# Kernel tuning notes

Measured on AMD Instinct MI355X. Metric: run time of the kernel, lower is better.

## Reference

```python
import math
import jax, jax.numpy as jnp
from jax import lax
import numpy as np

B, N, D, H, L, F = 128, 200, 128, 8, 3, 2048


def setup_inputs():
    key = jax.random.key(0)
    ks = jax.random.split(key, 24)
    g = lambda i, shape: (0.05 * jax.random.normal(ks[i], shape)).astype(jnp.float32)
    coords = jax.random.uniform(ks[0], (B, N, 2), dtype=jnp.float32)
    demands = jax.random.uniform(ks[1], (B, N), minval=1.0, maxval=10.0, dtype=jnp.float32)
    demands = demands.at[:, 0].set(0.0)  # depot demand = 0
    capacity = jnp.full((B,), 50.0, jnp.float32)
    return dict(
        coords=coords, demands_raw=demands, capacity_raw=capacity,
        embed_W=g(2, (D, 3)), embed_b=g(3, (D,)),
        Wqkv=g(4, (L, 3 * D, D)), bqkv=g(5, (L, 3 * D)),
        Wo=g(6, (L, D, D)), bo=g(7, (L, D)),
        W1=g(8, (L, F, D)), b1=g(9, (L, F)),
        W2=g(10, (L, D, F)), b2=g(11, (L, D)),
        ln1_g=jnp.ones((L, D), jnp.float32), ln1_b=jnp.zeros((L, D), jnp.float32),
        ln2_g=jnp.ones((L, D), jnp.float32), ln2_b=jnp.zeros((L, D), jnp.float32),
        Wq=g(12, (D, D)), Wk=g(13, (D, D)),
        Wcap=g(14, (D, 1)), bcap=g(15, (D,)),
        Wctx=g(16, (D, 3 * D)), bctx=g(17, (D,)),
    )


def _ln(x, g, b):
    m = x.mean(-1, keepdims=True)
    v = ((x - m) ** 2).mean(-1, keepdims=True)
    return (x - m) / jnp.sqrt(v + 1e-5) * g + b


def _forward(coords, demands_raw, capacity_raw, embed_W, embed_b, Wqkv, bqkv, Wo, bo,
             W1, b1, W2, b2, ln1_g, ln1_b, ln2_g, ln2_b, Wq, Wk, Wcap, bcap, Wctx, bctx):
    Bd, Nd, _ = coords.shape
    cap = capacity_raw.reshape(Bd, 1)
    demand_ratio = demands_raw / cap                       # (B,N)
    x = jnp.concatenate([coords, demand_ratio[..., None]], -1)  # (B,N,3)
    h = x @ embed_W.T + embed_b                            # (B,N,D)
    d = h.shape[-1]
    dh = d // H
    # --- transformer encoder (post-LN, relu FFN), eval mode (no dropout) ---
    for i in range(Wqkv.shape[0]):
        qkv = h @ Wqkv[i].T + bqkv[i]
        q, k, v = jnp.split(qkv, 3, -1)
        q = q.reshape(Bd, Nd, H, dh)
        k = k.reshape(Bd, Nd, H, dh)
        v = v.reshape(Bd, Nd, H, dh)
        s = jnp.einsum('bqhd,bkhd->bhqk', q, k) / math.sqrt(dh)
        a = jax.nn.softmax(s, -1)
        o = jnp.einsum('bhqk,bkhd->bqhd', a, v).reshape(Bd, Nd, d) @ Wo[i].T + bo[i]
        h = _ln(h + o, ln1_g[i], ln1_b[i])
        f = jax.nn.relu(h @ W1[i].T + b1[i]) @ W2[i].T + b2[i]
        h = _ln(h + f, ln2_g[i], ln2_b[i])
    global_ctx = h.mean(1)                                 # (B,D)
    kmat = h @ Wk.T                                        # K cache: static across steps
    sqrt_d = math.sqrt(d)
    max_steps = 2 * (Nd - 1) + 1
    ar = jnp.arange(Bd)

    def step(carry, _):
        current, visited, remaining, done, key = carry
        key, sk = jax.random.split(key)
        cur_h = h[ar, current]                             # (B,D)
        cap_h = remaining @ Wcap.T + bcap                  # (B,D)
        q_in = jnp.concatenate([cur_h, global_ctx, cap_h], -1)
        q = (q_in @ Wctx.T + bctx) @ Wq.T                  # (B,D)
        logits = (kmat * q[:, None, :]).sum(-1) / sqrt_d   # (B,N)
        infeasible = visited | (demand_ratio > remaining)
        feas_cust = (~visited[:, 1:]) & (demand_ratio[:, 1:] <= remaining)
        has_feas = feas_cust.any(1)
        all_served = visited[:, 1:].all(1)
        force_depot = all_served & (current != 0) & (~done)
        at_depot = (current == 0) & (~done)
        not_depot = (current != 0) & (~done)
        # prevent_early_return=True path
        depot_mask = (at_depot & has_feas) | (not_depot & has_feas & (~all_served))
        infeasible = infeasible.at[:, 0].set(infeasible[:, 0] | depot_mask)
        force_depot = force_depot | (not_depot & (~has_feas)) | done
        masked = jnp.where(infeasible, -1e9, logits)
        logp = jax.nn.log_softmax(masked, -1)
        sel = jax.random.categorical(sk, masked)           # sampling decode
        sel_logp = logp[ar, sel]
        sel = jnp.where(force_depot, 0, sel)
        sel_logp = jnp.where(force_depot, 0.0, sel_logp)
        is_depot = sel == 0
        take = demand_ratio[ar, sel][:, None]
        remaining = jnp.clip(jnp.where(is_depot[:, None], 1.0, remaining - take), 0.0, 1.0)
        visited = visited.at[ar, sel].set(visited[ar, sel] | (~is_depot))
        done = done | (visited[:, 1:].all(1) & (sel == 0))
        return (sel, visited, remaining, done, key), (sel, sel_logp)

    init = (jnp.zeros(Bd, jnp.int32), jnp.zeros((Bd, Nd), bool),
            jnp.ones((Bd, 1), coords.dtype), jnp.zeros(Bd, bool), jax.random.key(42))
    _, (acts, lps) = lax.scan(step, init, None, length=max_steps)
    path = jnp.concatenate([jnp.zeros((Bd, 1), jnp.int32), acts.T], 1)  # (B, 1+max_steps)
    logps = lps.sum(0)                                                  # (B,)
    return path, logps


def reference(coords, demands_raw, capacity_raw, embed_W, embed_b, Wqkv, bqkv, Wo, bo,
              W1, b1, W2, b2, ln1_g, ln1_b, ln2_g, ln2_b, Wq, Wk, Wcap, bcap, Wctx, bctx):
    return _forward(coords, demands_raw, capacity_raw, embed_W, embed_b, Wqkv, bqkv, Wo, bo,
                    W1, b1, W2, b2, ln1_g, ln1_b, ln2_g, ln2_b, Wq, Wk, Wcap, bcap, Wctx, bctx)
```

## Files before the change

### kernel.cpp

```cpp
#include <hip/hip_runtime.h>
#include <hip/hip_bf16.h>
#include <stdint.h>
#include <math.h>

#define NB 128
#define NN 200
#define ND 128
#define NH 8
#define DH 16
#define NL 3
#define NF 2048
#define NT (NB * NN)
#define NSTEP 399

__host__ __device__ inline void tf2x32(unsigned k0, unsigned k1, unsigned x0, unsigned x1,
                                       unsigned* o0, unsigned* o1) {
  unsigned ks[3] = {k0, k1, k0 ^ k1 ^ 0x1BD11BDAu};
  x0 += ks[0]; x1 += ks[1];
  const unsigned R[2][4] = {{13u, 15u, 26u, 6u}, {17u, 29u, 16u, 24u}};
#pragma unroll
  for (int i = 0; i < 5; ++i) {
#pragma unroll
    for (int j = 0; j < 4; ++j) {
      unsigned r = R[i & 1][j];
      x0 += x1;
      x1 = (x1 << r) | (x1 >> (32u - r));
      x1 ^= x0;
    }
    x0 += ks[(i + 1) % 3];
    x1 += ks[(i + 2) % 3] + (unsigned)(i + 1);
  }
  *o0 = x0; *o1 = x1;
}

__global__ void k_rng(unsigned* __restrict__ rng) {
  __shared__ unsigned ksh[2 * NSTEP];
  const int l = threadIdx.x;
  if (l == 0) {
    unsigned k0 = 0u, k1 = 42u;
    for (int t = 0; t < NSTEP; ++t) {
      ksh[2 * t] = k0; ksh[2 * t + 1] = k1;
      unsigned a0, a1;
      tf2x32(k0, k1, 0u, 0u, &a0, &a1);
      k0 = a0; k1 = a1;
    }
  }
  __syncthreads();
  for (int t = l; t < NSTEP; t += 64) {
    unsigned s0, s1;
    tf2x32(ksh[2 * t], ksh[2 * t + 1], 0u, 1u, &s0, &s1);
    rng[2 * t] = s0; rng[2 * t + 1] = s1;
  }
}

__global__ __launch_bounds__(256) void k_gum(const unsigned* __restrict__ rng, float* __restrict__ gum) {
  int idx = blockIdx.x * 256 + threadIdx.x;
  if (idx >= NSTEP * NT) return;
  int t = idx / NT, j = idx - t * NT;
  unsigned o0, o1;
  tf2x32(rng[2 * t], rng[2 * t + 1], 0u, (unsigned)j, &o0, &o1);
  unsigned bits = o0 ^ o1;
  float u01 = __uint_as_float((bits >> 9) | 0x3f800000u) - 1.0f;
  float uu = fmaxf(1.17549435082228751e-38f, u01);
  gum[idx] = (float)(-log(-log((double)uu)));
}

__global__ void k_tr(const float* __restrict__ src, float* __restrict__ dst, int R, int C) {
  int i = blockIdx.x * 256 + threadIdx.x;
  if (i >= R * C) return;
  int c = i / R, r = i - c * R;
  dst[i] = src[(size_t)r * C + c];
}

__global__ void k_trd(const float* __restrict__ src, double* __restrict__ dst, int R, int C) {
  int i = blockIdx.x * 256 + threadIdx.x;
  if (i >= R * C) return;
  int c = i / R, r = i - c * R;
  dst[i] = (double)src[(size_t)r * C + c];
}

__global__ void k_embed(const float* __restrict__ coords, const float* __restrict__ dem,
                        const float* __restrict__ cap, const float* __restrict__ eW,
                        const float* __restrict__ eb, float* __restrict__ h, float* __restrict__ dr) {
  int gid = blockIdx.x * blockDim.x + threadIdx.x;
  int t = gid >> 7, d = gid & 127;
  int b = t / NN;
  float drv = dem[t] / cap[b];
  double acc = (double)eW[d * 3] * (double)coords[2 * t]
             + (double)eW[d * 3 + 1] * (double)coords[2 * t + 1]
             + (double)eW[d * 3 + 2] * (double)drv;
  h[gid] = (float)acc + eb[d];
  if (d == 0) dr[t] = drv;
}

#define QT 8
__global__ __launch_bounds__(384) void k_qkv(const float* __restrict__ h, const double* __restrict__ WT,
                                             const float* __restrict__ bias, float* __restrict__ qkv) {
  const int t0 = blockIdx.x * QT, j = threadIdx.x;
  __shared__ double hsh[ND][QT];
  for (int idx = j; idx < ND * QT; idx += 384) {
    int t = idx & 7, k = idx >> 3;
    hsh[k][t] = (double)h[(size_t)(t0 + t) * ND + k];
  }
  __syncthreads();
  double acc[QT];
#pragma unroll
  for (int t = 0; t < QT; ++t) acc[t] = 0.0;
  for (int k = 0; k < ND; ++k) {
    double w = WT[(size_t)k * 384 + j];
#pragma unroll
    for (int t = 0; t < QT; ++t) acc[t] += w * hsh[k][t];
  }
  float bv = bias[j];
#pragma unroll
  for (int t = 0; t < QT; ++t)
    qkv[(size_t)(t0 + t) * 384 + j] = (float)acc[t] + bv;
}

__global__ __launch_bounds__(256) void k_attn(const float* __restrict__ qkv, float* __restrict__ att) {
  const int b = blockIdx.x / NH, hh = blockIdx.x % NH, tid = threadIdx.x;
  const int lane = tid & 63, w = tid >> 6;
  __shared__ float qsh[NN][DH + 1];
  __shared__ float ksh[NN][DH + 1];
  __shared__ float vsh[NN][DH + 1];
  __shared__ float ashw[4][NN + 8];
  for (int idx = tid; idx < NN * DH; idx += 256) {
    int n = idx / DH, d2 = idx % DH;
    size_t base = (size_t)(b * NN + n) * 384 + hh * DH + d2;
    qsh[n][d2] = qkv[base];
    ksh[n][d2] = qkv[base + ND];
    vsh[n][d2] = qkv[base + 2 * ND];
  }
  __syncthreads();
  const int dd = lane & 15, q4 = lane >> 4;
  for (int qn = w; qn < NN; qn += 4) {
    double qv[DH];
#pragma unroll
    for (int d = 0; d < DH; ++d) qv[d] = (double)qsh[qn][d];
    float sf[4];
#pragma unroll
    for (int s = 0; s < 4; ++s) {
      int n = lane + 64 * s;
      if (n < NN) {
        double a = 0.0;
#pragma unroll
        for (int d = 0; d < DH; ++d) a += qv[d] * (double)ksh[n][d];
        sf[s] = (float)a / 4.0f;
      } else sf[s] = -3.0e38f;
    }
    float m = fmaxf(fmaxf(sf[0], sf[1]), fmaxf(sf[2], sf[3]));
    for (int off = 1; off < 64; off <<= 1) m = fmaxf(m, __shfl_xor(m, off, 64));
    double e[4];
    double esum = 0.0;
#pragma unroll
    for (int s = 0; s < 4; ++s) {
      int n = lane + 64 * s;
      e[s] = (n < NN) ? exp((double)(sf[s] - m)) : 0.0;
      esum += e[s];
    }
    for (int off = 1; off < 64; off <<= 1) esum += __shfl_xor(esum, off, 64);
#pragma unroll
    for (int s = 0; s < 4; ++s) {
      int n = lane + 64 * s;
      if (n < NN) ashw[w][n] = (float)(e[s] / esum);
    }
    double o = 0.0;
    for (int i = 0; i < 50; ++i) {
      int n = q4 * 50 + i;
      o += (double)ashw[w][n] * (double)vsh[n][dd];
    }
    o += __shfl_xor(o, 16, 64);
    o += __shfl_xor(o, 32, 64);
    if (lane < DH)
      att[(size_t)(b * NN + qn) * ND + hh * DH + lane] = (float)o;
  }
}

#define OT 4
__global__ __launch_bounds__(128) void k_oln(const float* __restrict__ att, const double* __restrict__ WoT,
                                             const float* __restrict__ bo, const float* __restrict__ g,
                                             const float* __restrict__ bb, float* __restrict__ h) {
  const int t0 = blockIdx.x * OT, d = threadIdx.x;
  __shared__ double ash[ND][OT];
  __shared__ float xsh[OT][ND];
  __shared__ float mred[OT], sred[OT];
  for (int idx = d; idx < ND * OT; idx += 128) {
    int t = idx & 3, k = idx >> 2;
    ash[k][t] = (double)att[(size_t)(t0 + t) * ND + k];
  }
  __syncthreads();
  double acc[OT];
#pragma unroll
  for (int t = 0; t < OT; ++t) acc[t] = 0.0;
  for (int k = 0; k < ND; ++k) {
    double w = WoT[(size_t)k * ND + d];
#pragma unroll
    for (int t = 0; t < OT; ++t) acc[t] += w * ash[k][t];
  }
  float bv = bo[d];
#pragma unroll
  for (int t = 0; t < OT; ++t) {
    float o = (float)acc[t] + bv;
    xsh[t][d] = h[(size_t)(t0 + t) * ND + d] + o;
  }
  __syncthreads();
  if (d < OT) {
    double sv = 0.0;
    for (int k = 0; k < ND; ++k) sv += (double)xsh[d][k];
    float m = (float)(sv / 128.0);
    double sq = 0.0;
    for (int k = 0; k < ND; ++k) { float tf = xsh[d][k] - m; sq += (double)tf * (double)tf; }
    mred[d] = m;
    sred[d] = sqrtf((float)(sq / 128.0) + 1e-5f);
  }
  __syncthreads();
#pragma unroll
  for (int t = 0; t < OT; ++t) {
    float tf = xsh[t][d] - mred[t];
    h[(size_t)(t0 + t) * ND + d] = tf / sred[t] * g[d] + bb[d];
  }
}

#define FT 8
#define JC 1024
__global__ __launch_bounds__(256) void k_ffn(float* __restrict__ h, const double* __restrict__ W1T,
                                             const float* __restrict__ b1, const float* __restrict__ W2T,
                                             const float* __restrict__ b2, const float* __restrict__ g,
                                             const float* __restrict__ bb) {
  const int t0 = blockIdx.x * FT, tid = threadIdx.x;
  __shared__ double hsh[ND][FT];
  __shared__ double fsh_raw[FT * JC / 2];
  __shared__ float xsh[FT][ND];
  __shared__ float mred[FT], sred[FT];
  float* fshf = (float*)fsh_raw;
  for (int idx = tid; idx < ND * FT; idx += 256) {
    int t = idx & 7, k = idx >> 3;
    hsh[k][t] = (double)h[(size_t)(t0 + t) * ND + k];
  }
  __syncthreads();
  const int jg = tid >> 5, dl = tid & 31;
  double acc2[4][FT];
#pragma unroll
  for (int a = 0; a < 4; ++a)
#pragma unroll
    for (int t = 0; t < FT; ++t) acc2[a][t] = 0.0;
  for (int c = 0; c < 2; ++c) {
    {
      const int j0 = tid * 4;
      double acc[4][FT];
#pragma unroll
      for (int a = 0; a < 4; ++a)
#pragma unroll
        for (int t = 0; t < FT; ++t) acc[a][t] = 0.0;
      const double* wp0 = W1T + (size_t)c * JC + j0;
      double2 wa = *(const double2*)wp0;
      double2 wb = *(const double2*)(wp0 + 2);
      for (int k = 0; k < ND; ++k) {
        double wd[4] = {wa.x, wa.y, wb.x, wb.y};
        const double* wn = W1T + (size_t)((k + 1) & 127) * NF + c * JC + j0;
        wa = *(const double2*)wn;
        wb = *(const double2*)(wn + 2);
        double hv[FT];
#pragma unroll
        for (int t = 0; t < FT; ++t) hv[t] = hsh[k][t];
#pragma unroll
        for (int a = 0; a < 4; ++a)
#pragma unroll
          for (int t = 0; t < FT; ++t) acc[a][t] += wd[a] * hv[t];
      }
#pragma unroll
      for (int a = 0; a < 4; ++a) {
        float bv = b1[c * JC + j0 + a];
#pragma unroll
        for (int t = 0; t < FT; ++t) {
          float f = (float)acc[a][t] + bv;
          fshf[t * JC + j0 + a] = fmaxf(f, 0.0f);
        }
      }
    }
    __syncthreads();
    {
      float4 wv = *(const float4*)(W2T + (size_t)(c * JC + ((jg << 7) | (jg & 127))) * ND + (dl << 2));
      for (int i = 0; i < 128; ++i) {
        int jj = (jg << 7) | ((i + jg) & 127);
        int jn = (jg << 7) | ((i + 1 + jg) & 127);
        float4 wnext = *(const float4*)(W2T + (size_t)(c * JC + jn) * ND + (dl << 2));
        double fv[FT];
#pragma unroll
        for (int t = 0; t < FT; ++t) fv[t] = (double)fshf[t * JC + jj];
        double wd[4] = {(double)wv.x, (double)wv.y, (double)wv.z, (double)wv.w};
#pragma unroll
        for (int a = 0; a < 4; ++a)
#pragma unroll
          for (int t = 0; t < FT; ++t) acc2[a][t] += wd[a] * fv[t];
        wv = wnext;
      }
    }
    __syncthreads();
  }
  double* red = fsh_raw;
  for (int half = 0; half < 2; ++half) {
    if (half) __syncthreads();
#pragma unroll
    for (int a = 0; a < 4; ++a)
#pragma unroll
      for (int t = 0; t < 4; ++t)
        red[((jg * 4 + t) << 7) + (dl << 2) + a] = acc2[a][half * 4 + t];
    __syncthreads();
    for (int idx = tid; idx < ND * 4; idx += 256) {
      int t = idx >> 7, d = idx & 127;
      double s = 0.0;
#pragma unroll
      for (int jg2 = 0; jg2 < 8; ++jg2) s += red[((jg2 * 4 + t) << 7) + d];
      float o = (float)s + b2[d];
      int tt = half * 4 + t;
      xsh[tt][d] = (float)hsh[d][tt] + o;
    }
  }
  __syncthreads();
  if (tid < FT) {
    double sv = 0.0;
    for (int d = 0; d < ND; ++d) sv += (double)xsh[tid][d];
    float m = (float)(sv / 128.0);
    double sq = 0.0;
    for (int d = 0; d < ND; ++d) { float tf = xsh[tid][d] - m; sq += (double)tf * (double)tf; }
    mred[tid] = m;
    sred[tid] = sqrtf((float)(sq / 128.0) + 1e-5f);
  }
  __syncthreads();
  for (int idx = tid; idx < ND * FT; idx += 256) {
    int d = idx & 127, t = idx >> 7;
    float tf = xsh[t][d] - mred[t];
    h[(size_t)(t0 + t) * ND + d] = tf / sred[t] * g[d] + bb[d];
  }
}

__global__ __launch_bounds__(128) void k_gctx(const float* __restrict__ h, float* __restrict__ gctx) {
  int b = blockIdx.x, d = threadIdx.x;
  double acc = 0.0;
  for (int n = 0; n < NN; ++n) acc += (double)h[(size_t)(b * NN + n) * ND + d];
  gctx[b * ND + d] = (float)(acc / 200.0);
}

#define KT 8
__global__ __launch_bounds__(128) void k_kmat(const float* __restrict__ h, const double* __restrict__ WkT,
                                              float* __restrict__ kmat) {
  const int t0 = blockIdx.x * KT, d = threadIdx.x;
  __shared__ double hsh[ND][KT];
  for (int idx = d; idx < ND * KT; idx += 128) {
    int t = idx & 7, k = idx >> 3;
    hsh[k][t] = (double)h[(size_t)(t0 + t) * ND + k];
  }
  __syncthreads();
  double acc[KT];
#pragma unroll
  for (int t = 0; t < KT; ++t) acc[t] = 0.0;
  for (int k = 0; k < ND; ++k) {
    double w = WkT[(size_t)k * ND + d];
#pragma unroll
    for (int t = 0; t < KT; ++t) acc[t] += w * hsh[k][t];
  }
#pragma unroll
  for (int t = 0; t < KT; ++t)
    kmat[(size_t)(t0 + t) * ND + d] = (float)acc[t];
}

__global__ __launch_bounds__(128) void k_prep1(const float* __restrict__ Wctx, const float* __restrict__ bcap,
                                               const float* __restrict__ Wcap, const float* __restrict__ bctx,
                                               double* __restrict__ t1, double* __restrict__ wu) {
  int k = threadIdx.x;
  double a = 0.0, c = 0.0;
  for (int m = 0; m < ND; ++m) {
    double wc = (double)Wctx[(size_t)k * 384 + 256 + m];
    a += wc * (double)bcap[m];
    c += wc * (double)Wcap[m];
  }
  t1[k] = a + (double)bctx[k];
  wu[k] = c;
}

__global__ __launch_bounds__(128) void k_M(const float* __restrict__ Wq, const float* __restrict__ Wctx,
                                           double* __restrict__ M) {
  int d = blockIdx.x, j = threadIdx.x;
  double acc = 0.0;
  for (int k = 0; k < ND; ++k)
    acc += (double)Wq[(size_t)d * ND + k] * (double)Wctx[(size_t)k * 384 + j];
  M[(size_t)d * ND + j] = acc;
}

__global__ __launch_bounds__(128) void k_u(const float* __restrict__ Wq, const double* __restrict__ wu,
                                           double* __restrict__ u) {
  int d = threadIdx.x;
  double acc = 0.0;
  for (int k = 0; k < ND; ++k) acc += (double)Wq[(size_t)d * ND + k] * wu[k];
  u[d] = acc;
}

__global__ __launch_bounds__(128) void k_t2(const float* __restrict__ Wctx, const float* __restrict__ gctx,
                                            double* __restrict__ t2) {
  int b = blockIdx.x, k = threadIdx.x;
  double acc = 0.0;
  for (int m = 0; m < ND; ++m)
    acc += (double)Wctx[(size_t)k * 384 + 128 + m] * (double)gctx[b * ND + m];
  t2[(size_t)b * ND + k] = acc;
}

__global__ __launch_bounds__(128) void k_vb(const float* __restrict__ Wq, const double* __restrict__ t2,
                                            const double* __restrict__ t1, double* __restrict__ vb) {
  int b = blockIdx.x, d = threadIdx.x;
  double acc = 0.0;
  for (int k = 0; k < ND; ++k)
    acc += (double)Wq[(size_t)d * ND + k] * (t2[(size_t)b * ND + k] + t1[k]);
  vb[(size_t)b * ND + d] = acc;
}

__global__ __launch_bounds__(256) void k_c01(const float* __restrict__ kmat, const double* __restrict__ vb,
                                             const double* __restrict__ u, float* __restrict__ c0, float* __restrict__ c1) {
  int t = blockIdx.x * 256 + threadIdx.x;
  if (t >= NT) return;
  int b = t / NN;
  double a0 = 0.0, a1 = 0.0;
  for (int d = 0; d < ND; ++d) {
    double km = (double)kmat[(size_t)t * ND + d];
    a0 += km * vb[(size_t)b * ND + d];
    a1 += km * u[d];
  }
  c0[t] = (float)a0;
  c1[t] = (float)a1;
}

__global__ __launch_bounds__(128) void k_KM(const float* __restrict__ kmat, const double* __restrict__ M,
                                            float* __restrict__ KMT) {
  const int t0 = blockIdx.x * KT, j = threadIdx.x;
  const int b = t0 / NN, toff = t0 % NN;
  __shared__ double ksh[ND][KT];
  for (int idx = j; idx < ND * KT; idx += 128) {
    int t = idx & 7, k = idx >> 3;
    ksh[k][t] = (double)kmat[(size_t)(t0 + t) * ND + k];
  }
  __syncthreads();
  double acc[KT];
#pragma unroll
  for (int t = 0; t < KT; ++t) acc[t] = 0.0;
  for (int d = 0; d < ND; ++d) {
    double m = M[(size_t)d * ND + j];
#pragma unroll
    for (int t = 0; t < KT; ++t) acc[t] += ksh[d][t] * m;
  }
#pragma unroll
  for (int t = 0; t < KT; ++t)
    KMT[(size_t)b * ND * NN + (size_t)j * NN + toff + t] = (float)acc[t];
}

#define PC 8
__global__ __launch_bounds__(256) void k_P(const float* __restrict__ KMT, const float* __restrict__ h,
                                           float* __restrict__ P) {
  const int blk = blockIdx.x;
  const int b = blk / 25, c0 = (blk % 25) * PC;
  const int tid = threadIdx.x;
  __shared__ double h8[ND][PC];
  for (int idx = tid; idx < ND * PC; idx += 256) {
    int t = idx & 7, j = idx >> 3;
    h8[j][t] = (double)h[(size_t)(b * NN + c0 + t) * ND + j];
  }
  __syncthreads();
  if (tid < NN) {
    double acc[PC];
#pragma unroll
    for (int t = 0; t < PC; ++t) acc[t] = 0.0;
    const float* kb = KMT + (size_t)b * ND * NN + tid;
    for (int j = 0; j < ND; ++j) {
      double km = (double)kb[(size_t)j * NN];
#pragma unroll
      for (int t = 0; t < PC; ++t) acc[t] += km * h8[j][t];
    }
#pragma unroll
    for (int t = 0; t < PC; ++t)
      P[(size_t)(b * NN + c0 + t) * NN + tid] = (float)acc[t];
  }
}

__global__ __launch_bounds__(64) void k_decode(const float* __restrict__ P, const float* __restrict__ c0,
                                               const float* __restrict__ c1, const float* __restrict__ dr,
                                               const float* __restrict__ gum, float* __restrict__ out) {
  __shared__ float Psh[NN * NN];
  const int b = blockIdx.x, l = threadIdx.x;
  {
    const float4* src = (const float4*)(P + (size_t)b * NN * NN);
    float4* dst = (float4*)Psh;
    for (int i = l; i < (NN * NN) / 4; i += 64) dst[i] = src[i];
  }
  float drs4[4], c04[4], c14[4];
  int vis4[4];
#pragma unroll
  for (int s = 0; s < 4; ++s) {
    int n = l + 64 * s;
    bool valid = n < NN;
    drs4[s] = valid ? dr[b * NN + n] : 1e9f;
    c04[s] = valid ? c0[b * NN + n] : 0.0f;
    c14[s] = valid ? c1[b * NN + n] : 0.0f;
    vis4[s] = valid ? 0 : 1;
  }
  int cur = 0, done = 0;
  float rem = 1.0f, lpsum = 0.0f;
  if (l == 0) out[(size_t)b * 400] = 0.0f;
  __syncthreads();
  const float SQD = 11.3137084989847603f;
  float gv4[4];
#pragma unroll
  for (int s = 0; s < 4; ++s) {
    int n = l + 64 * s;
    gv4[s] = (n < NN) ? gum[(size_t)0 * NT + b * NN + n] : 0.0f;
  }
  for (int t = 0; t < NSTEP; ++t) {
    float gn4[4];
    if (t + 1 < NSTEP) {
      const float* grow = gum + (size_t)(t + 1) * NT + b * NN;
#pragma unroll
      for (int s = 0; s < 4; ++s) {
        int n = l + 64 * s;
        gn4[s] = (n < NN) ? grow[n] : 0.0f;
      }
    }
    const float* Prow = Psh + cur * NN;
    float Pv4[4];
#pragma unroll
    for (int s = 0; s < 4; ++s) {
      int n = l + 64 * s;
      Pv4[s] = (n < NN) ? Prow[n] : 0.0f;
    }
    bool lf = false, lns = false;
#pragma unroll
    for (int s = 0; s < 4; ++s) {
      int n = l + 64 * s;
      if (n >= 1 && n < NN && !vis4[s]) {
        lns = true;
        if (drs4[s] <= rem) lf = true;
      }
    }
    const int has_feas = (__ballot(lf) != 0ULL);
    const int all_served = (__ballot(lns) == 0ULL);
    const bool at_depot = (cur == 0) && !done, not_depot = (cur != 0) && !done;
    const bool depot_mask = (at_depot && has_feas) || (not_depot && has_feas && !all_served);
    float msk[4], sc[4];
#pragma unroll
    for (int s = 0; s < 4; ++s) {
      int n = l + 64 * s;
      if (n < NN) {
        double sd = (double)Pv4[s] + (double)c04[s] + (double)rem * (double)c14[s];
        float logit = (float)sd / SQD;
        bool infn = vis4[s] || (drs4[s] > rem) || (n == 0 && depot_mask);
        msk[s] = infn ? -1e9f : logit;
        sc[s] = msk[s] + gv4[s];
      } else {
        msk[s] = -3.0e38f;
        sc[s] = -3.0e38f;
      }
    }
    float bs = sc[0]; int bn = l; float bmsk = msk[0]; float mx = msk[0];
#pragma unroll
    for (int s = 1; s < 4; ++s) {
      int n = l + 64 * s;
      if (sc[s] > bs) { bs = sc[s]; bn = n; bmsk = msk[s]; }
      mx = fmaxf(mx, msk[s]);
    }
    for (int off = 1; off < 64; off <<= 1) {
      float os = __shfl_xor(bs, off, 64);
      int on = __shfl_xor(bn, off, 64);
      float ob = __shfl_xor(bmsk, off, 64);
      float om = __shfl_xor(mx, off, 64);
      if (os > bs || (os == bs && on < bn)) { bs = os; bn = on; bmsk = ob; }
      mx = fmaxf(mx, om);
    }
    float e = 0.0f;
#pragma unroll
    for (int s = 0; s < 4; ++s) e += expf(msk[s] - mx);
    for (int off = 1; off < 64; off <<= 1) e += __shfl_xor(e, off, 64);
    int sel = bn;
    float slp = (bmsk - mx) - logf(e);
    bool force = (all_served && cur != 0 && !done) || (not_depot && !has_feas) || done;
    if (force) { sel = 0; slp = 0.0f; }
    if (l == 0) out[(size_t)b * 400 + 1 + t] = (float)sel;
    lpsum += slp;
    bool isd = (sel == 0);
    float cand = drs4[sel >> 6];
    float take = __shfl(cand, sel & 63, 64);
    float nr = isd ? 1.0f : (rem - take);
    rem = fminf(fmaxf(nr, 0.0f), 1.0f);
    if (!isd && (sel & 63) == l) vis4[sel >> 6] = 1;
    if (all_served && sel == 0) done = 1;
    cur = sel;
#pragma unroll
    for (int s = 0; s < 4; ++s) gv4[s] = gn4[s];
  }
  if (l == 0) out[(size_t)NB * 400 + b] = lpsum;
}

extern "C" void kernel_launch(void* const* d_in, const int* in_sizes, int n_in,
                              void* d_out, int out_size, void* d_ws, size_t ws_size,
                              hipStream_t stream) {
  (void)in_sizes; (void)n_in; (void)out_size; (void)ws_size;
  const float* coords = (const float*)d_in[0];
  const float* dem    = (const float*)d_in[1];
  const float* cap    = (const float*)d_in[2];
  const float* eW     = (const float*)d_in[3];
  const float* eb     = (const float*)d_in[4];
  const float* Wqkv   = (const float*)d_in[5];
  const float* bqkv   = (const float*)d_in[6];
  const float* Wo     = (const float*)d_in[7];
  const float* bo     = (const float*)d_in[8];
  const float* W1     = (const float*)d_in[9];
  const float* b1     = (const float*)d_in[10];
  const float* W2     = (const float*)d_in[11];
  const float* b2     = (const float*)d_in[12];
  const float* ln1g   = (const float*)d_in[13];
  const float* ln1b   = (const float*)d_in[14];
  const float* ln2g   = (const float*)d_in[15];
  const float* ln2b   = (const float*)d_in[16];
  const float* Wq     = (const float*)d_in[17];
  const float* Wk     = (const float*)d_in[18];
  const float* Wcap   = (const float*)d_in[19];
  const float* bcap   = (const float*)d_in[20];
  const float* Wctx   = (const float*)d_in[21];
  const float* bctx   = (const float*)d_in[22];

  char* ws = (char*)d_ws;
  size_t off = 0;
  auto take = [&](size_t bytes) -> void* {
    void* p = ws + off;
    off += (bytes + 255) & ~(size_t)255;
    return p;
  };
  float* dr   = (float*)take((size_t)NT * 4);
  float* c0   = (float*)take((size_t)NT * 4);
  float* c1   = (float*)take((size_t)NT * 4);
  float* P    = (float*)take((size_t)NB * NN * NN * 4);
  unsigned* rng = (unsigned*)take((size_t)NSTEP * 2 * 4);
  float* h    = (float*)take((size_t)NT * ND * 4);
  float* qkv  = (float*)take((size_t)NT * 384 * 4);
  float* att  = (float*)take((size_t)NT * ND * 4);
  float* kmat = (float*)take((size_t)NT * ND * 4);
  float* gctx = (float*)take((size_t)NB * ND * 4);
  double* M   = (double*)take((size_t)ND * ND * 8);
  double* u   = (double*)take((size_t)ND * 8);
  double* t1  = (double*)take((size_t)ND * 8);
  double* wu  = (double*)take((size_t)ND * 8);
  double* t2  = (double*)take((size_t)NB * ND * 8);
  double* vb  = (double*)take((size_t)NB * ND * 8);
  double* W1T   = (double*)take((size_t)NL * NF * ND * 8);
  float*  W2T   = (float*)take((size_t)NL * NF * ND * 4);
  double* WqkvT = (double*)take((size_t)NL * 384 * ND * 8);
  double* WoT   = (double*)take((size_t)NL * ND * ND * 8);
  double* WkT   = (double*)take((size_t)ND * ND * 8);
  float* KMT = qkv;
  float* gum = h;

  k_rng<<<1, 64, 0, stream>>>(rng);
  for (int i = 0; i < NL; ++i) {
    k_trd<<<(NF * ND + 255) / 256, 256, 0, stream>>>(W1 + (size_t)i * NF * ND, W1T + (size_t)i * NF * ND, NF, ND);
    k_tr<<<(NF * ND + 255) / 256, 256, 0, stream>>>(W2 + (size_t)i * ND * NF, W2T + (size_t)i * ND * NF, ND, NF);
    k_trd<<<(384 * ND + 255) / 256, 256, 0, stream>>>(Wqkv + (size_t)i * 384 * ND, WqkvT + (size_t)i * 384 * ND, 384, ND);
    k_trd<<<(ND * ND + 255) / 256, 256, 0, stream>>>(Wo + (size_t)i * ND * ND, WoT + (size_t)i * ND * ND, ND, ND);
  }
  k_trd<<<(ND * ND + 255) / 256, 256, 0, stream>>>(Wk, WkT, ND, ND);
  k_embed<<<(NT * ND) / 256, 256, 0, stream>>>(coords, dem, cap, eW, eb, h, dr);
  for (int i = 0; i < NL; ++i) {
    k_qkv<<<NT / QT, 384, 0, stream>>>(h, WqkvT + (size_t)i * 384 * ND, bqkv + (size_t)i * 384, qkv);
    k_attn<<<NB * NH, 256, 0, stream>>>(qkv, att);
    k_oln<<<NT / OT, 128, 0, stream>>>(att, WoT + (size_t)i * ND * ND, bo + (size_t)i * ND,
                                       ln1g + (size_t)i * ND, ln1b + (size_t)i * ND, h);
    k_ffn<<<NT / FT, 256, 0, stream>>>(h, W1T + (size_t)i * NF * ND, b1 + (size_t)i * NF,
                                       W2T + (size_t)i * ND * NF, b2 + (size_t)i * ND,
                                       ln2g + (size_t)i * ND, ln2b + (size_t)i * ND);
  }
  k_gctx<<<NB, 128, 0, stream>>>(h, gctx);
  k_kmat<<<NT / KT, 128, 0, stream>>>(h, WkT, kmat);
  k_prep1<<<1, 128, 0, stream>>>(Wctx, bcap, Wcap, bctx, t1, wu);
  k_M<<<ND, 128, 0, stream>>>(Wq, Wctx, M);
  k_u<<<1, 128, 0, stream>>>(Wq, wu, u);
  k_t2<<<NB, 128, 0, stream>>>(Wctx, gctx, t2);
  k_vb<<<NB, 128, 0, stream>>>(Wq, t2, t1, vb);
  k_c01<<<NT / 256, 256, 0, stream>>>(kmat, vb, u, c0, c1);
  k_KM<<<NT / KT, 128, 0, stream>>>(kmat, M, KMT);
  k_P<<<NB * 25, 256, 0, stream>>>(KMT, h, P);
  k_gum<<<(NSTEP * NT + 255) / 256, 256, 0, stream>>>(rng, gum);
  k_decode<<<NB, 64, 0, stream>>>(P, c0, c1, dr, gum, (float*)d_out);
}
```

Baseline: 4.747 ms.

## Widen FFN kernel to 512 threads with smaller per-thread accumulators

Doubles the FFN block to 512 threads, with launch bounds that ask for four blocks per CU. Each thread now computes 2 hidden columns in the first GEMM and 4 tokens × 4 outputs in the second, which cuts its double-precision accumulator registers to raise occupancy. The hidden-state tile moves to float shared memory read with vector loads, and the explicit software prefetch of weights is dropped. The catch is fewer independent FMAs per thread, less latency hiding from prefetch, and more threads sharing the same shared-memory budget.

```diff
diff --git a/kernel.cpp b/kernel.cpp
--- a/kernel.cpp
+++ b/kernel.cpp
@@ -223,98 +223,99 @@
 
 #define FT 8
 #define JC 1024
-__global__ __launch_bounds__(256) void k_ffn(float* __restrict__ h, const double* __restrict__ W1T,
-                                             const float* __restrict__ b1, const float* __restrict__ W2T,
-                                             const float* __restrict__ b2, const float* __restrict__ g,
-                                             const float* __restrict__ bb) {
+__global__ __launch_bounds__(512, 4) void k_ffn(float* __restrict__ h, const double* __restrict__ W1T,
+                                                const float* __restrict__ b1, const float* __restrict__ W2T,
+                                                const float* __restrict__ b2, const float* __restrict__ g,
+                                                const float* __restrict__ bb) {
   const int t0 = blockIdx.x * FT, tid = threadIdx.x;
-  __shared__ double hsh[ND][FT];
+  __shared__ float hshf[ND][FT];
   __shared__ double fsh_raw[FT * JC / 2];
   __shared__ float xsh[FT][ND];
   __shared__ float mred[FT], sred[FT];
   float* fshf = (float*)fsh_raw;
-  for (int idx = tid; idx < ND * FT; idx += 256) {
-    int t = idx & 7, k = idx >> 3;
-    hsh[k][t] = (double)h[(size_t)(t0 + t) * ND + k];
-  }
-  __syncthreads();
-  const int jg = tid >> 5, dl = tid & 31;
-  double acc2[4][FT];
+  for (int idx = tid; idx < ND * FT; idx += 512) {
+    int k = idx & 127, t = idx >> 7;
+    hshf[k][t] = h[(size_t)(t0 + t) * ND + k];
+  }
+  __syncthreads();
+  const int jg = tid >> 6;
+  const int dl = tid & 63;
+  const int th = dl >> 5;
+  const int dlo = dl & 31, d0 = dlo << 2;
+  double acc2[4][4];
 #pragma unroll
   for (int a = 0; a < 4; ++a)
 #pragma unroll
-    for (int t = 0; t < FT; ++t) acc2[a][t] = 0.0;
+    for (int t = 0; t < 4; ++t) acc2[a][t] = 0.0;
   for (int c = 0; c < 2; ++c) {
     {
-      const int j0 = tid * 4;
-      double acc[4][FT];
-#pragma unroll
-      for (int a = 0; a < 4; ++a)
+      const int j0 = tid * 2;
+      double acc[2][FT];
+#pragma unroll
+      for (int a = 0; a < 2; ++a)
 #pragma unroll
         for (int t = 0; t < FT; ++t) acc[a][t] = 0.0;
-      const double* wp0 = W1T + (size_t)c * JC + j0;
-      double2 wa = *(const double2*)wp0;
-      double2 wb = *(const double2*)(wp0 + 2);
+      const double* wrow = W1T + (size_t)c * JC + j0;
       for (int k = 0; k < ND; ++k) {
-        double wd[4] = {wa.x, wa.y, wb.x, wb.y};
-        const double* wn = W1T + (size_t)((k + 1) & 127) * NF + c * JC + j0;
-        wa = *(const double2*)wn;
-        wb = *(const double2*)(wn + 2);
-        double hv[FT];
-#pragma unroll
-        for (int t = 0; t < FT; ++t) hv[t] = hsh[k][t];
-#pragma unroll
-        for (int a = 0; a < 4; ++a)
-#pragma unroll
-          for (int t = 0; t < FT; ++t) acc[a][t] += wd[a] * hv[t];
-      }
-#pragma unroll
-      for (int a = 0; a < 4; ++a) {
-        float bv = b1[c * JC + j0 + a];
+        double2 w = *(const double2*)(wrow + (size_t)k * NF);
+        float4 ha = *(const float4*)&hshf[k][0];
+        float4 hb = *(const float4*)&hshf[k][4];
+        float hf[FT] = {ha.x, ha.y, ha.z, ha.w, hb.x, hb.y, hb.z, hb.w};
 #pragma unroll
         for (int t = 0; t < FT; ++t) {
-          float f = (float)acc[a][t] + bv;
-          fshf[t * JC + j0 + a] = fmaxf(f, 0.0f);
+          double hv = (double)hf[t];
+          acc[0][t] += w.x * hv;
+          acc[1][t] += w.y * hv;
         }
       }
+      float bv0 = b1[c * JC + j0];
+      float bv1 = b1[c * JC + j0 + 1];
+#pragma unroll
+      for (int t = 0; t < FT; ++t) {
+        float f0 = (float)acc[0][t] + bv0;
+        float f1 = (float)acc[1][t] + bv1;
+        float2 fw;
+        fw.x = fmaxf(f0, 0.0f);
+        fw.y = fmaxf(f1, 0.0f);
+        *(float2*)&fshf[t * JC + j0] = fw;
+      }
     }
     __syncthreads();
-    {
-      float4 wv = *(const float4*)(W2T + (size_t)(c * JC + ((jg << 7) | (jg & 127))) * ND + (dl << 2));
-      for (int i = 0; i < 128; ++i) {
-        int jj = (jg << 7) | ((i + jg) & 127);
-        int jn = (jg << 7) | ((i + 1 + jg) & 127);
-        float4 wnext = *(const float4*)(W2T + (size_t)(c * JC + jn) * ND + (dl << 2));
-        double fv[FT];
-#pragma unroll
-        for (int t = 0; t < FT; ++t) fv[t] = (double)fshf[t * JC + jj];
-        double wd[4] = {(double)wv.x, (double)wv.y, (double)wv.z, (double)wv.w};
-#pragma unroll
-        for (int a = 0; a < 4; ++a)
-#pragma unroll
-          for (int t = 0; t < FT; ++t) acc2[a][t] += wd[a] * fv[t];
-        wv = wnext;
-      }
+    for (int i = 0; i < 128; ++i) {
+      int jj = (jg << 7) | ((i + jg) & 127);
+      int j = c * JC + jj;
+      float4 wv = *(const float4*)(W2T + (size_t)j * ND + d0);
+      double fv[4];
+#pragma unroll
+      for (int t = 0; t < 4; ++t) fv[t] = (double)fshf[(th * 4 + t) * JC + jj];
+      double wd[4] = {(double)wv.x, (double)wv.y, (double)wv.z, (double)wv.w};
+#pragma unroll
+      for (int a = 0; a < 4; ++a)
+#pragma unroll
+        for (int t = 0; t < 4; ++t) acc2[a][t] += wd[a] * fv[t];
     }
     __syncthreads();
   }
   double* red = fsh_raw;
   for (int half = 0; half < 2; ++half) {
     if (half) __syncthreads();
-#pragma unroll
-    for (int a = 0; a < 4; ++a)
-#pragma unroll
-      for (int t = 0; t < 4; ++t)
-        red[((jg * 4 + t) << 7) + (dl << 2) + a] = acc2[a][half * 4 + t];
+    if (th == half) {
+#pragma unroll
+      for (int a = 0; a < 4; ++a)
+#pragma unroll
+        for (int t = 0; t < 4; ++t)
+          red[((jg * 4 + t) << 7) + d0 + a] = acc2[a][t];
+    }
     __syncthreads();
-    for (int idx = tid; idx < ND * 4; idx += 256) {
+    {
+      int idx = tid;
       int t = idx >> 7, d = idx & 127;
       double s = 0.0;
 #pragma unroll
       for (int jg2 = 0; jg2 < 8; ++jg2) s += red[((jg2 * 4 + t) << 7) + d];
       float o = (float)s + b2[d];
       int tt = half * 4 + t;
-      xsh[tt][d] = (float)hsh[d][tt] + o;
+      xsh[tt][d] = hshf[d][tt] + o;
     }
   }
   __syncthreads();
@@ -328,7 +329,7 @@
     sred[tid] = sqrtf((float)(sq / 128.0) + 1e-5f);
   }
   __syncthreads();
-  for (int idx = tid; idx < ND * FT; idx += 256) {
+  for (int idx = tid; idx < ND * FT; idx += 512) {
     int d = idx & 127, t = idx >> 7;
     float tf = xsh[t][d] - mred[t];
     h[(size_t)(t0 + t) * ND + d] = tf / sred[t] * g[d] + bb[d];
@@ -669,7 +670,7 @@
     k_attn<<<NB * NH, 256, 0, stream>>>(qkv, att);
     k_oln<<<NT / OT, 128, 0, stream>>>(att, WoT + (size_t)i * ND * ND, bo + (size_t)i * ND,
                                        ln1g + (size_t)i * ND, ln1b + (size_t)i * ND, h);
-    k_ffn<<<NT / FT, 256, 0, stream>>>(h, W1T + (size_t)i * NF * ND, b1 + (size_t)i * NF,
+    k_ffn<<<NT / FT, 512, 0, stream>>>(h, W1T + (size_t)i * NF * ND, b1 + (size_t)i * NF,
                                        W2T + (size_t)i * ND * NF, b2 + (size_t)i * ND,
                                        ln2g + (size_t)i * ND, ln2b + (size_t)i * ND);
   }
```

Result: slower. 5.064 ms (+6.7%).
